# Optimization experiments

Hardware: AMD Instinct MI355X
Metric: run time of the kernel (lower is better)

The kernel has to match this reference:

```python
import jax, jax.numpy as jnp
import numpy as np

N_HEAD = 16

def apply_rope(t, cos, sin):
    # t: [B, H, T, hd]; cos/sin: [T, hd//2] -> broadcast [1,1,T,hd//2]
    hd = t.shape[-1]
    t1, t2 = t[..., : hd // 2], t[..., hd // 2 :]
    c = cos[None, None, :, :]
    s = sin[None, None, :, :]
    return jnp.concatenate([t1 * c - t2 * s, t1 * s + t2 * c], axis=-1)

def setup_inputs() -> dict:
    key = jax.random.key(0)
    k1, k2, k3, k4, k5 = jax.random.split(key, 5)
    B, T, C = 2, 2048, 2048
    hd = C // N_HEAD
    x = jax.random.normal(k1, (B, T, C), dtype=jnp.float32)
    cos = jax.random.uniform(k2, (T, hd // 2), dtype=jnp.float32)
    sin = jax.random.uniform(k3, (T, hd // 2), dtype=jnp.float32)
    W_attn = jax.random.normal(k4, (C, 3 * C), dtype=jnp.float32) * (1.0 / np.sqrt(C))
    W_proj = jax.random.normal(k5, (C, C), dtype=jnp.float32) * (1.0 / np.sqrt(C))
    return {"x": x, "cos": cos, "sin": sin, "W_attn": W_attn, "W_proj": W_proj}

def reference(x, cos, sin, W_attn, W_proj):
    B, T, C = x.shape
    hd = C // N_HEAD
    qkv = jnp.einsum("btc,cd->btd", x, W_attn)  # [B,T,3C]
    q, k, v = jnp.split(qkv, 3, axis=-1)
    # [B,T,C] -> [B,H,T,hd]
    def to_heads(t):
        return t.reshape(B, T, N_HEAD, hd).transpose(0, 2, 1, 3)
    q, k, v = to_heads(q), to_heads(k), to_heads(v)
    q = apply_rope(q, cos[:T], sin[:T])
    k = apply_rope(k, cos[:T], sin[:T])
    scale = 1.0 / np.sqrt(hd).astype(np.float32)
    scores = jnp.einsum("bhqd,bhkd->bhqk", q, k) * scale
    causal = jnp.tril(jnp.ones((T, T), dtype=bool))
    scores = jnp.where(causal[None, None], scores, jnp.finfo(scores.dtype).min)
    attn = jax.nn.softmax(scores, axis=-1)
    y = jnp.einsum("bhqk,bhkd->bhqd", attn, v)  # [B,H,T,hd]
    y = y.transpose(0, 2, 1, 3).reshape(B, T, C)
    return jnp.einsum("btc,cd->btd", y, W_proj)
```

## Files before the change

kernel.cpp:

```cpp
#include <hip/hip_runtime.h>
#include <stdint.h>

typedef unsigned short u16;
typedef __bf16 v8bf __attribute__((ext_vector_type(8)));
typedef float f32x4 __attribute__((ext_vector_type(4)));

#define MFMA16(a, b, c) __builtin_amdgcn_mfma_f32_16x16x32_bf16((a), (b), (c), 0, 0, 0)

typedef const __attribute__((address_space(1))) uint32_t* gp32;
typedef __attribute__((address_space(3))) uint32_t* lp32;
#define ASYNC16(g, l) __builtin_amdgcn_global_load_lds((gp32)(const void*)(g), (lp32)(void*)(l), 16, 0, 0)

__device__ __forceinline__ u16 f2bf(float f) {
  union { float f; uint32_t u; } v; v.f = f;
  uint32_t r = v.u + 0x7fffu + ((v.u >> 16) & 1u);
  return (u16)(r >> 16);
}
__device__ __forceinline__ float bf2f(u16 h) {
  union { uint32_t u; float f; } v; v.u = ((uint32_t)h) << 16;
  return v.f;
}

__device__ __forceinline__ int swK(int r, int lc) {
  return r * 128 + (((lc ^ (r & 7)) & 15) << 3);
}
__device__ __forceinline__ int swV(int r, int lc) {
  return r * 64 + (((lc ^ (r & 7)) & 7) << 3);
}

__device__ __forceinline__ void transpose_tile(const float* __restrict__ in,
                                               u16* __restrict__ out, int R, int Cc,
                                               int bx, int by, int tid,
                                               u16 (*tile)[34]) {
  int c0 = bx * 32, r0 = by * 32;
  int tx = tid & 31, ty = tid >> 5;
#pragma unroll
  for (int i = 0; i < 32; i += 8)
    tile[ty + i][tx] = f2bf(in[(size_t)(r0 + ty + i) * Cc + c0 + tx]);
  __syncthreads();
#pragma unroll
  for (int i = 0; i < 32; i += 8)
    out[(size_t)(c0 + ty + i) * R + r0 + tx] = tile[tx][ty + i];
}

__global__ __launch_bounds__(256) void prep_kernel(const float* __restrict__ x,
                                                   u16* __restrict__ xb,
                                                   const float* __restrict__ Wa,
                                                   u16* __restrict__ WaT,
                                                   const float* __restrict__ Wp,
                                                   u16* __restrict__ WpT) {
  __shared__ u16 tile[32][34];
  int bid = blockIdx.x;
  int tid = threadIdx.x;
  if (bid < 4096) {
    int i = (bid * 256 + tid) * 8;
    float4 a = *(const float4*)(x + i);
    float4 b = *(const float4*)(x + i + 4);
    uint4 o;
    o.x = (uint32_t)f2bf(a.x) | ((uint32_t)f2bf(a.y) << 16);
    o.y = (uint32_t)f2bf(a.z) | ((uint32_t)f2bf(a.w) << 16);
    o.z = (uint32_t)f2bf(b.x) | ((uint32_t)f2bf(b.y) << 16);
    o.w = (uint32_t)f2bf(b.z) | ((uint32_t)f2bf(b.w) << 16);
    *(uint4*)(xb + i) = o;
  } else if (bid < 4096 + 12288) {
    int t = bid - 4096;
    transpose_tile(Wa, WaT, 2048, 6144, t % 192, t / 192, tid, tile);
  } else {
    int t = bid - 16384;
    transpose_tile(Wp, WpT, 2048, 2048, t & 63, t >> 6, tid, tile);
  }
}

template <typename OutT>
__global__ __launch_bounds__(256) void gemm_bt(const u16* __restrict__ A,
                                               const u16* __restrict__ Bt,
                                               OutT* __restrict__ C, int M, int N, int K) {
  __shared__ u16 As[128 * 64];
  __shared__ u16 Bs[128 * 64];
  int tid = threadIdx.x;
  int wave = tid >> 6, lane = tid & 63, quad = lane >> 4, l16 = lane & 15;
  int wr = wave >> 1, wc = wave & 1;
  int m0 = blockIdx.y * 128, n0 = blockIdx.x * 128;
  f32x4 acc[4][4] = {};
  int lrow = lane >> 3, lk = lane & 7;
  int lc = lk ^ lrow;
  const u16* Ab = A + (size_t)m0 * K;
  const u16* Bb = Bt + (size_t)n0 * K;

  for (int k0 = 0; k0 < K; k0 += 64) {
#pragma unroll
    for (int j = 0; j < 4; ++j) {
      int rbase = wave * 32 + j * 8;
      int row = rbase + lrow;
      ASYNC16(Ab + (size_t)row * K + k0 + lc * 8, &As[rbase * 64]);
      ASYNC16(Bb + (size_t)row * K + k0 + lc * 8, &Bs[rbase * 64]);
    }
    __syncthreads();
#pragma unroll
    for (int ks = 0; ks < 2; ++ks) {
      v8bf af[4], bfr[4];
#pragma unroll
      for (int t = 0; t < 4; ++t) {
        af[t]  = *(const v8bf*)&As[swV(wr * 64 + t * 16 + l16, ks * 4 + quad)];
        bfr[t] = *(const v8bf*)&Bs[swV(wc * 64 + t * 16 + l16, ks * 4 + quad)];
      }
#pragma unroll
      for (int mt = 0; mt < 4; ++mt)
#pragma unroll
        for (int nt = 0; nt < 4; ++nt)
          acc[mt][nt] = MFMA16(af[mt], bfr[nt], acc[mt][nt]);
    }
    __syncthreads();
  }
#pragma unroll
  for (int mt = 0; mt < 4; ++mt)
#pragma unroll
    for (int nt = 0; nt < 4; ++nt) {
      int row = m0 + wr * 64 + mt * 16 + quad * 4;
      int col = n0 + wc * 64 + nt * 16 + l16;
#pragma unroll
      for (int r = 0; r < 4; ++r) {
        float v = acc[mt][nt][r];
        if constexpr (sizeof(OutT) == 2)
          C[(size_t)(row + r) * N + col] = (OutT)f2bf(v);
        else
          C[(size_t)(row + r) * N + col] = v;
      }
    }
}

__global__ __launch_bounds__(256) void rope_repack(const u16* __restrict__ qkv,
                                                   const float* __restrict__ cosp,
                                                   const float* __restrict__ sinp,
                                                   u16* __restrict__ qh, u16* __restrict__ kh,
                                                   u16* __restrict__ vt) {
  __shared__ u16 tile[128 * 130];
  const int T = 2048, C3 = 6144;
  const float QSCL = 0.08838834764831845f * 1.4426950408889634f;
  int t0 = blockIdx.x * 128;
  int bh = blockIdx.y, b = bh >> 4, h = bh & 15;
  int tid = threadIdx.x;
#pragma unroll 2
  for (int i = 0; i < 32; ++i) {
    int e = i * 256 + tid;
    int tl = e >> 6, j = e & 63;
    int t = t0 + tl;
    size_t base = (size_t)(b * T + t) * C3 + h * 128;
    float c = cosp[t * 64 + j], s = sinp[t * 64 + j];
    float q1 = bf2f(qkv[base + j]),        q2 = bf2f(qkv[base + 64 + j]);
    float k1 = bf2f(qkv[base + 2048 + j]), k2 = bf2f(qkv[base + 2048 + 64 + j]);
    size_t o = ((size_t)bh * T + t) * 128;
    qh[o + j]      = f2bf((q1 * c - q2 * s) * QSCL);
    qh[o + 64 + j] = f2bf((q1 * s + q2 * c) * QSCL);
    kh[o + j]      = f2bf(k1 * c - k2 * s);
    kh[o + 64 + j] = f2bf(k1 * s + k2 * c);
  }
#pragma unroll 2
  for (int i = 0; i < 32; ++i) {
    int e = i * 256 + tid;
    int tl = e >> 6, dc = (e & 63) * 2;
    size_t base = (size_t)(b * T + t0 + tl) * C3 + 4096 + h * 128;
    *(uint32_t*)&tile[tl * 130 + dc] = *(const uint32_t*)&qkv[base + dc];
  }
  __syncthreads();
#pragma unroll 2
  for (int i = 0; i < 32; ++i) {
    int e = i * 256 + tid;
    int d = e >> 6, tp = (e & 63) * 2;
    uint32_t v = (uint32_t)tile[tp * 130 + d] | ((uint32_t)tile[(tp + 1) * 130 + d] << 16);
    *(uint32_t*)&vt[((size_t)bh * 128 + d) * T + t0 + tp] = v;
  }
}

__global__ __launch_bounds__(512) void flash_attn(const u16* __restrict__ qh,
                                                  const u16* __restrict__ kh,
                                                  const u16* __restrict__ vt,
                                                  u16* __restrict__ yh) {
  __shared__ u16 Ks[2][64 * 128];
  __shared__ u16 Vs[2][128 * 64];
  __shared__ u16 Pb[128 * 64];
  const int T = 2048, HD = 128;
  int tid = threadIdx.x;
  int wave = tid >> 6, lane = tid & 63, quad = lane >> 4, l16 = lane & 15;
  int bh = blockIdx.y, b = bh >> 4, h = bh & 15;
  const u16* qb = qh + (size_t)bh * T * HD;
  const u16* kb = kh + (size_t)bh * T * HD;
  const u16* vb = vt + (size_t)bh * HD * T;
  int krow_off = lane >> 4, kchunk = lane & 15;
  int vrow_off = lane >> 3, vchunk = lane & 7;

  for (int tp = 0; tp < 2; ++tp) {
    int qt = tp ? 15 - (int)blockIdx.x : (int)blockIdx.x;
    int q0 = qt * 128;
    int n_it = 2 * qt + 2;

    v8bf qf[4];
#pragma unroll
    for (int ks = 0; ks < 4; ++ks)
      qf[ks] = *(const v8bf*)&qb[(size_t)(q0 + wave * 16 + l16) * HD + ks * 32 + quad * 8];

    f32x4 acc[8] = {};
    float rs_p[4] = {};
    uint4 vreg[2];

#pragma unroll
    for (int j = 0; j < 2; ++j) {
      int rbase = wave * 8 + j * 4;
      int r = rbase + krow_off;
      int lc = kchunk ^ (r & 7);
      ASYNC16(kb + (size_t)r * HD + lc * 8, &Ks[0][rbase * 128]);
    }
#pragma unroll
    for (int j = 0; j < 2; ++j) {
      int row = wave * 16 + j * 8 + vrow_off;
      int lc = vchunk ^ (row & 7);
      vreg[j] = *(const uint4*)&vb[(size_t)row * T + lc * 8];
    }
#pragma unroll
    for (int j = 0; j < 2; ++j) {
      int row = wave * 16 + j * 8 + vrow_off;
      *(uint4*)&Vs[0][row * 64 + vchunk * 8] = vreg[j];
    }
    __syncthreads();

    for (int it = 0; it < n_it; ++it) {
      int c = it & 1;

      if (it + 1 < n_it) {
        int kv0n = (it + 1) * 64;
#pragma unroll
        for (int j = 0; j < 2; ++j) {
          int rbase = wave * 8 + j * 4;
          int r = rbase + krow_off;
          int lc = kchunk ^ (r & 7);
          ASYNC16(kb + (size_t)(kv0n + r) * HD + lc * 8, &Ks[1 - c][rbase * 128]);
        }
#pragma unroll
        for (int j = 0; j < 2; ++j) {
          int row = wave * 16 + j * 8 + vrow_off;
          int lc = vchunk ^ (row & 7);
          vreg[j] = *(const uint4*)&vb[(size_t)row * T + kv0n + lc * 8];
        }
      }

      f32x4 s[4] = {};
#pragma unroll
      for (int ks = 0; ks < 4; ++ks)
#pragma unroll
        for (int nt = 0; nt < 4; ++nt) {
          v8bf kf = *(const v8bf*)&Ks[c][swK(nt * 16 + l16, ks * 4 + quad)];
          s[nt] = MFMA16(qf[ks], kf, s[nt]);
        }

      if (it >= 2 * qt) {
        int kv0 = it * 64;
#pragma unroll
        for (int r = 0; r < 4; ++r) {
          int row = q0 + wave * 16 + quad * 4 + r;
#pragma unroll
          for (int nt = 0; nt < 4; ++nt)
            if (kv0 + nt * 16 + l16 > row) s[nt][r] = -1e30f;
        }
      }

#pragma unroll
      for (int nt = 0; nt < 4; ++nt)
#pragma unroll
        for (int r = 0; r < 4; ++r) {
          float p = __builtin_exp2f(s[nt][r]);
          rs_p[r] += p;
          int row = wave * 16 + quad * 4 + r;
          int col = nt * 16 + l16;
          Pb[row * 64 + ((((col >> 3) ^ (row & 7)) & 7) << 3) + (col & 7)] = f2bf(p);
        }

#pragma unroll
      for (int ks = 0; ks < 2; ++ks) {
        v8bf pa = *(const v8bf*)&Pb[swV(wave * 16 + l16, ks * 4 + quad)];
#pragma unroll
        for (int dt = 0; dt < 8; ++dt) {
          v8bf vf = *(const v8bf*)&Vs[c][swV(dt * 16 + l16, ks * 4 + quad)];
          acc[dt] = MFMA16(pa, vf, acc[dt]);
        }
      }

      if (it + 1 < n_it) {
#pragma unroll
        for (int j = 0; j < 2; ++j) {
          int row = wave * 16 + j * 8 + vrow_off;
          *(uint4*)&Vs[1 - c][row * 64 + vchunk * 8] = vreg[j];
        }
      }

      __syncthreads();
    }

#pragma unroll
    for (int r = 0; r < 4; ++r) {
      float rsv = rs_p[r];
      rsv += __shfl_xor(rsv, 1);
      rsv += __shfl_xor(rsv, 2);
      rsv += __shfl_xor(rsv, 4);
      rsv += __shfl_xor(rsv, 8);
      float inv = 1.f / rsv;
      int t = q0 + wave * 16 + quad * 4 + r;
#pragma unroll
      for (int dt = 0; dt < 8; ++dt)
        yh[(size_t)(b * T + t) * 2048 + h * 128 + dt * 16 + l16] = f2bf(acc[dt][r] * inv);
    }
  }
}

extern "C" void kernel_launch(void* const* d_in, const int* in_sizes, int n_in,
                              void* d_out, int out_size, void* d_ws, size_t ws_size,
                              hipStream_t stream) {
  const float* x    = (const float*)d_in[0];
  const float* cosp = (const float*)d_in[1];
  const float* sinp = (const float*)d_in[2];
  const float* Wa   = (const float*)d_in[3];
  const float* Wp   = (const float*)d_in[4];
  float* out = (float*)d_out;

  char* ws = (char*)d_ws;
  u16* xb  = (u16*)(ws);
  u16* WaT = (u16*)(ws + (size_t)(16 << 20));
  u16* WpT = (u16*)(ws + (size_t)(40 << 20));
  u16* qkv = (u16*)(ws + (size_t)(48 << 20));
  u16* qh  = (u16*)(ws + (size_t)(96 << 20));
  u16* kh  = (u16*)(ws + (size_t)(112 << 20));
  u16* vt  = (u16*)(ws + (size_t)(128 << 20));
  u16* yh  = (u16*)(ws + (size_t)(144 << 20));

  prep_kernel<<<20480, 256, 0, stream>>>(x, xb, Wa, WaT, Wp, WpT);
  gemm_bt<u16><<<dim3(48, 32), 256, 0, stream>>>(xb, WaT, qkv, 4096, 6144, 2048);
  rope_repack<<<dim3(16, 32), 256, 0, stream>>>(qkv, cosp, sinp, qh, kh, vt);
  flash_attn<<<dim3(8, 32), 512, 0, stream>>>(qh, kh, vt, yh);
  gemm_bt<float><<<dim3(16, 32), 256, 0, stream>>>(yh, WpT, out, 4096, 2048, 2048);
}
```

Measured before the change: 407.2 us.

## Fuse RoPE and head repacking into QKV GEMM epilogue

Replaces the separate QKV GEMM and rope_repack kernels with a single GEMM whose epilogue stages the 128x128 bf16 output tile in shared memory. It then applies RoPE and the Q scale for Q/K tiles, or transposes V tiles, and writes straight into head-major buffers. This removes the round trip of the 48 MB intermediate qkv tensor through global memory and one kernel launch. The epilogue adds shared-memory staging and uses narrower global stores for V, and the fused kernel may not match the old GEMM's inner loop.

```diff
diff --git a/kernel.cpp b/kernel.cpp
--- a/kernel.cpp
+++ b/kernel.cpp
@@ -129,46 +129,96 @@
     }
 }
 
-__global__ __launch_bounds__(256) void rope_repack(const u16* __restrict__ qkv,
-                                                   const float* __restrict__ cosp,
-                                                   const float* __restrict__ sinp,
-                                                   u16* __restrict__ qh, u16* __restrict__ kh,
-                                                   u16* __restrict__ vt) {
-  __shared__ u16 tile[128 * 130];
-  const int T = 2048, C3 = 6144;
-  const float QSCL = 0.08838834764831845f * 1.4426950408889634f;
-  int t0 = blockIdx.x * 128;
-  int bh = blockIdx.y, b = bh >> 4, h = bh & 15;
+__global__ __launch_bounds__(256) void gemm_qkv_rope(const u16* __restrict__ A,
+                                                     const u16* __restrict__ Bt,
+                                                     const float* __restrict__ cosp,
+                                                     const float* __restrict__ sinp,
+                                                     u16* __restrict__ qh,
+                                                     u16* __restrict__ kh,
+                                                     u16* __restrict__ vt) {
+  const int K = 2048, T = 2048;
+  __shared__ u16 smem[128 * 130];
+  u16* As = smem;
+  u16* Bs = smem + 128 * 64;
   int tid = threadIdx.x;
-#pragma unroll 2
-  for (int i = 0; i < 32; ++i) {
-    int e = i * 256 + tid;
-    int tl = e >> 6, j = e & 63;
-    int t = t0 + tl;
-    size_t base = (size_t)(b * T + t) * C3 + h * 128;
-    float c = cosp[t * 64 + j], s = sinp[t * 64 + j];
-    float q1 = bf2f(qkv[base + j]),        q2 = bf2f(qkv[base + 64 + j]);
-    float k1 = bf2f(qkv[base + 2048 + j]), k2 = bf2f(qkv[base + 2048 + 64 + j]);
-    size_t o = ((size_t)bh * T + t) * 128;
-    qh[o + j]      = f2bf((q1 * c - q2 * s) * QSCL);
-    qh[o + 64 + j] = f2bf((q1 * s + q2 * c) * QSCL);
-    kh[o + j]      = f2bf(k1 * c - k2 * s);
-    kh[o + 64 + j] = f2bf(k1 * s + k2 * c);
-  }
-#pragma unroll 2
-  for (int i = 0; i < 32; ++i) {
-    int e = i * 256 + tid;
-    int tl = e >> 6, dc = (e & 63) * 2;
-    size_t base = (size_t)(b * T + t0 + tl) * C3 + 4096 + h * 128;
-    *(uint32_t*)&tile[tl * 130 + dc] = *(const uint32_t*)&qkv[base + dc];
-  }
+  int wave = tid >> 6, lane = tid & 63, quad = lane >> 4, l16 = lane & 15;
+  int wr = wave >> 1, wc = wave & 1;
+  int m0 = blockIdx.y * 128, n0 = blockIdx.x * 128;
+  f32x4 acc[4][4] = {};
+  int lrow = lane >> 3, lk = lane & 7;
+  int lc = lk ^ lrow;
+  const u16* Ab = A + (size_t)m0 * K;
+  const u16* Bb = Bt + (size_t)n0 * K;
+
+  for (int k0 = 0; k0 < K; k0 += 64) {
+#pragma unroll
+    for (int j = 0; j < 4; ++j) {
+      int rbase = wave * 32 + j * 8;
+      int row = rbase + lrow;
+      ASYNC16(Ab + (size_t)row * K + k0 + lc * 8, &As[rbase * 64]);
+      ASYNC16(Bb + (size_t)row * K + k0 + lc * 8, &Bs[rbase * 64]);
+    }
+    __syncthreads();
+#pragma unroll
+    for (int ks = 0; ks < 2; ++ks) {
+      v8bf af[4], bfr[4];
+#pragma unroll
+      for (int t = 0; t < 4; ++t) {
+        af[t]  = *(const v8bf*)&As[swV(wr * 64 + t * 16 + l16, ks * 4 + quad)];
+        bfr[t] = *(const v8bf*)&Bs[swV(wc * 64 + t * 16 + l16, ks * 4 + quad)];
+      }
+#pragma unroll
+      for (int mt = 0; mt < 4; ++mt)
+#pragma unroll
+        for (int nt = 0; nt < 4; ++nt)
+          acc[mt][nt] = MFMA16(af[mt], bfr[nt], acc[mt][nt]);
+    }
+    __syncthreads();
+  }
+
+#pragma unroll
+  for (int mt = 0; mt < 4; ++mt)
+#pragma unroll
+    for (int nt = 0; nt < 4; ++nt) {
+      int rloc = wr * 64 + mt * 16 + quad * 4;
+      int cloc = wc * 64 + nt * 16 + l16;
+#pragma unroll
+      for (int r = 0; r < 4; ++r)
+        smem[(rloc + r) * 130 + cloc] = f2bf(acc[mt][nt][r]);
+    }
   __syncthreads();
-#pragma unroll 2
-  for (int i = 0; i < 32; ++i) {
-    int e = i * 256 + tid;
-    int d = e >> 6, tp = (e & 63) * 2;
-    uint32_t v = (uint32_t)tile[tp * 130 + d] | ((uint32_t)tile[(tp + 1) * 130 + d] << 16);
-    *(uint32_t*)&vt[((size_t)bh * 128 + d) * T + t0 + tp] = v;
+
+  int sec = (int)blockIdx.x >> 4;
+  int h   = (int)blockIdx.x & 15;
+  int b   = m0 >> 11;
+  int t0  = m0 & 2047;
+  int bh  = b * 16 + h;
+
+  if (sec < 2) {
+    u16* dst = sec ? kh : qh;
+    const float QSCL = 0.08838834764831845f * 1.4426950408889634f;
+    float scl = sec ? 1.0f : QSCL;
+    int j = tid & 63, tl0 = tid >> 6;
+#pragma unroll 4
+    for (int i = 0; i < 32; ++i) {
+      int tl = i * 4 + tl0;
+      int t  = t0 + tl;
+      float c = cosp[t * 64 + j], s = sinp[t * 64 + j];
+      float x1 = bf2f(smem[tl * 130 + j]);
+      float x2 = bf2f(smem[tl * 130 + 64 + j]);
+      size_t o = ((size_t)bh * T + t) * 128;
+      dst[o + j]      = f2bf((x1 * c - x2 * s) * scl);
+      dst[o + 64 + j] = f2bf((x1 * s + x2 * c) * scl);
+    }
+  } else {
+    int l = tid & 63, w = tid >> 6;
+#pragma unroll 4
+    for (int i = 0; i < 32; ++i) {
+      int d = i * 4 + w;
+      size_t o = ((size_t)bh * 128 + d) * T + t0;
+      vt[o + l]      = smem[l * 130 + d];
+      vt[o + 64 + l] = smem[(64 + l) * 130 + d];
+    }
   }
 }
 
@@ -325,15 +375,13 @@
   u16* xb  = (u16*)(ws);
   u16* WaT = (u16*)(ws + (size_t)(16 << 20));
   u16* WpT = (u16*)(ws + (size_t)(40 << 20));
-  u16* qkv = (u16*)(ws + (size_t)(48 << 20));
-  u16* qh  = (u16*)(ws + (size_t)(96 << 20));
-  u16* kh  = (u16*)(ws + (size_t)(112 << 20));
-  u16* vt  = (u16*)(ws + (size_t)(128 << 20));
-  u16* yh  = (u16*)(ws + (size_t)(144 << 20));
+  u16* qh  = (u16*)(ws + (size_t)(48 << 20));
+  u16* kh  = (u16*)(ws + (size_t)(64 << 20));
+  u16* vt  = (u16*)(ws + (size_t)(80 << 20));
+  u16* yh  = (u16*)(ws + (size_t)(96 << 20));
 
   prep_kernel<<<20480, 256, 0, stream>>>(x, xb, Wa, WaT, Wp, WpT);
-  gemm_bt<u16><<<dim3(48, 32), 256, 0, stream>>>(xb, WaT, qkv, 4096, 6144, 2048);
-  rope_repack<<<dim3(16, 32), 256, 0, stream>>>(qkv, cosp, sinp, qh, kh, vt);
+  gemm_qkv_rope<<<dim3(48, 32), 256, 0, stream>>>(xb, WaT, cosp, sinp, qh, kh, vt);
   flash_attn<<<dim3(8, 32), 512, 0, stream>>>(qh, kh, vt, yh);
   gemm_bt<float><<<dim3(16, 32), 256, 0, stream>>>(yh, WpT, out, 4096, 2048, 2048);
 }
```

Measured after the change: 396.0 us. -2.8%, faster.
